# Performance work log

Hardware: AMD Instinct MI355X
Metric: run time of the kernel (lower is better)

Reference implementation:

```python
import jax, jax.numpy as jnp
import numpy as np

B, C, H, W = 16, 512, 64, 64


def setup_inputs() -> dict:
    key = jax.random.key(0)
    k1, k2 = jax.random.split(key)
    img_feat = jax.random.normal(k1, (B, C, H, W), dtype=jnp.float32)
    text_feat = jax.random.normal(k2, (B, C, H, W), dtype=jnp.float32)
    gamma = jnp.zeros((1,), dtype=jnp.float32)
    return {"img_feat": img_feat, "text_feat": text_feat, "gamma": gamma}


def reference(img_feat, text_feat, gamma):
    b, c, h, w = img_feat.shape
    q = img_feat.reshape(b, c, h * w)          # [B, C, HW]
    kv = text_feat.reshape(b, c, h * w)        # [B, C, HW]
    # channel-attention map: [B, C, C]
    attn = jnp.einsum('bcn,bdn->bcd', q, kv)
    attn = jax.nn.softmax(attn, axis=-1)
    info = jnp.einsum('bcd,bdn->bcn', attn, kv).reshape(b, c, h, w)
    return gamma * info + img_feat
```

## Files before the change

### kernel.cpp

```cpp
#include <hip/hip_runtime.h>
#include <hip/hip_bf16.h>


constexpr int NB = 16;
constexpr int NC = 512;
constexpr int NHW = 4096;
constexpr int QKSPLIT = 2;

typedef float f32x4 __attribute__((ext_vector_type(4)));
typedef __bf16 bf16x4 __attribute__((ext_vector_type(4)));
typedef __bf16 bf16x8 __attribute__((ext_vector_type(8)));

__device__ __forceinline__ void gload16(const void* g, void* l) {
  __builtin_amdgcn_global_load_lds(
      (const __attribute__((address_space(1))) void*)g,
      (__attribute__((address_space(3))) void*)l, 16, 0, 0);
}

template <int SPLITS>
__global__ __launch_bounds__(512) void gemm_qk(const float* __restrict__ Af,
                                               const __bf16* __restrict__ B,
                                               float* __restrict__ Dp) {
  __shared__ __bf16 sA[2][128 * 64];
  __shared__ __bf16 sB[2][128 * 64];

  const int t = threadIdx.x;
  const int lane = t & 63;
  const int wave = t >> 6;
  const int wr = wave >> 2;
  const int wc = wave & 3;

  constexpr int NWG = 16 * NB * SPLITS;
  constexpr int QX = NWG / 8;
  int flat = blockIdx.x + 4 * (blockIdx.y + 4 * blockIdx.z);
  flat = (flat & 7) * QX + (flat >> 3);
  const int bx = flat & 3;
  const int by = (flat >> 2) & 3;
  const int bz = flat >> 4;
  const int batch = bz / SPLITS;
  const int split = bz % SPLITS;

  const int aRow0 = bx * 128;
  const int bRow0 = by * 128;
  constexpr int KSUB = NHW / SPLITS;
  constexpr int NT = KSUB / 64;
  const int kBeg = split * KSUB;

  const int rl = lane >> 3;
  const int csrc = ((lane & 7) ^ rl) * 8;
  const __bf16* Bbase = B + (long)batch * NC * NHW +
                        (long)(bRow0 + wave * 16 + rl) * NHW + csrc + kBeg;
  const int ldsOff = wave * 16 * 64;

  const int c4 = (t & 15) * 4;
  const int rb = t >> 4;
  const float* Abase =
      Af + (long)batch * NC * NHW + (long)(aRow0 + rb) * NHW + kBeg + c4;

  f32x4 ra[4];
  auto loadA = [&](int kof) {
#pragma unroll
    for (int i = 0; i < 4; ++i)
      ra[i] = *(const f32x4*)(Abase + kof + (long)(32 * i) * NHW);
  };
  auto writeA = [&](int buf) {
#pragma unroll
    for (int i = 0; i < 4; ++i) {
      const int r = rb + 32 * i;
      const int idx = r * 64 + (c4 ^ ((r & 7) << 3));
      bf16x4 h = {(__bf16)ra[i].x, (__bf16)ra[i].y, (__bf16)ra[i].z,
                  (__bf16)ra[i].w};
      *(bf16x4*)&sA[buf][idx] = h;
    }
  };
  auto stageB = [&](int buf, int kof) {
#pragma unroll
    for (int i = 0; i < 2; ++i)
      gload16(Bbase + kof + (long)(i * 8) * NHW, &sB[buf][ldsOff + i * 8 * 64]);
  };

  f32x4 acc[4][2] = {};
  auto compute_tile = [&](int buf) {
#pragma unroll
    for (int kk = 0; kk < 2; ++kk) {
      const int kb = kk * 32 + ((lane >> 4) << 3);
      bf16x8 af[4], bfr[2];
#pragma unroll
      for (int m = 0; m < 4; ++m) {
        const int r = wr * 64 + m * 16 + (lane & 15);
        af[m] = *(const bf16x8*)&sA[buf][r * 64 + (kb ^ ((r & 7) << 3))];
      }
#pragma unroll
      for (int n = 0; n < 2; ++n) {
        const int r = wc * 32 + n * 16 + (lane & 15);
        bfr[n] = *(const bf16x8*)&sB[buf][r * 64 + (kb ^ ((r & 7) << 3))];
      }
#pragma unroll
      for (int m = 0; m < 4; ++m)
#pragma unroll
        for (int n = 0; n < 2; ++n)
          acc[m][n] = __builtin_amdgcn_mfma_f32_16x16x32_bf16(
              af[m], bfr[n], acc[m][n], 0, 0, 0);
    }
  };

  loadA(0);
  stageB(0, 0);
  asm volatile("s_waitcnt vmcnt(2)" ::: "memory");
  writeA(0);
  asm volatile("s_waitcnt vmcnt(0) lgkmcnt(0)" ::: "memory");
  __builtin_amdgcn_s_barrier();

  int cur = 0;
#pragma unroll 1
  for (int tt = 0; tt < NT; ++tt) {
    const bool more = (tt + 1) < NT;
    if (more) {
      loadA((tt + 1) * 64);
      stageB(cur ^ 1, (tt + 1) * 64);
      asm volatile("" ::: "memory");
    }
    compute_tile(cur);
    if (more) {
      asm volatile("s_waitcnt vmcnt(2)" ::: "memory");
      writeA(cur ^ 1);
      asm volatile("s_waitcnt vmcnt(0) lgkmcnt(0)" ::: "memory");
      __builtin_amdgcn_s_barrier();
      cur ^= 1;
    }
  }

  float* D = Dp + ((long)split * NB + batch) * NC * NC;
  const int m0 = aRow0 + wr * 64;
  const int n0 = bRow0 + wc * 32;
#pragma unroll
  for (int m = 0; m < 4; ++m)
#pragma unroll
    for (int n = 0; n < 2; ++n) {
      const int row0 = m0 + m * 16 + ((lane >> 4) << 2);
      const int col = n0 + n * 16 + (lane & 15);
#pragma unroll
      for (int r = 0; r < 4; ++r)
        D[(long)(row0 + r) * NC + col] = acc[m][n][r];
    }
}

__global__ __launch_bounds__(256) void gemm_pv(const __bf16* __restrict__ A,
                                               const __bf16* __restrict__ B,
                                               const float* __restrict__ img,
                                               const float* __restrict__ gammap,
                                               float* __restrict__ outp) {
  __shared__ __bf16 sA[64 * 64];
  __shared__ __bf16 sB[128 * 64];

  const int t = threadIdx.x;
  const int lane = t & 63;
  const int wave = t >> 6;
  const int wr = wave >> 1;
  const int wc = wave & 1;

  constexpr int GX = NHW / 64;
  constexpr int NWG = GX * 4 * NB;
  constexpr int QX = NWG / 8;
  int flat = blockIdx.x + GX * (blockIdx.y + 4 * blockIdx.z);
  flat = (flat & 7) * QX + (flat >> 3);
  const int bx = flat & 63;
  const int by = (flat >> 6) & 3;
  const int batch = flat >> 8;

  const int aRow0 = bx * 64;
  const int bRow0 = by * 128;

  const int rl = lane >> 3;
  const int csrc = ((lane & 7) ^ rl) * 8;
  const __bf16* Abase =
      A + (long)batch * NHW * NC + (long)(aRow0 + wave * 16 + rl) * NC + csrc;
  const int ldsOffA = wave * 16 * 64;
  const __bf16* Bbase =
      B + (long)batch * NC * NC + (long)(bRow0 + wave * 32 + rl) * NC + csrc;
  const int ldsOffB = wave * 32 * 64;

  f32x4 acc[2][4] = {};

#pragma unroll 1
  for (int k0 = 0; k0 < NC; k0 += 64) {
#pragma unroll
    for (int i = 0; i < 2; ++i)
      gload16(Abase + k0 + (long)(i * 8) * NC, &sA[ldsOffA + i * 8 * 64]);
#pragma unroll
    for (int i = 0; i < 4; ++i)
      gload16(Bbase + k0 + (long)(i * 8) * NC, &sB[ldsOffB + i * 8 * 64]);
    __syncthreads();
#pragma unroll
    for (int kk = 0; kk < 2; ++kk) {
      const int kb = kk * 32 + ((lane >> 4) << 3);
      bf16x8 af[2], bfr[4];
#pragma unroll
      for (int m = 0; m < 2; ++m) {
        const int r = wr * 32 + m * 16 + (lane & 15);
        af[m] = *(const bf16x8*)&sA[r * 64 + (kb ^ ((r & 7) << 3))];
      }
#pragma unroll
      for (int n = 0; n < 4; ++n) {
        const int r = wc * 64 + n * 16 + (lane & 15);
        bfr[n] = *(const bf16x8*)&sB[r * 64 + (kb ^ ((r & 7) << 3))];
      }
#pragma unroll
      for (int m = 0; m < 2; ++m)
#pragma unroll
        for (int n = 0; n < 4; ++n)
          acc[m][n] = __builtin_amdgcn_mfma_f32_16x16x32_bf16(
              af[m], bfr[n], acc[m][n], 0, 0, 0);
    }
    __syncthreads();
  }

  const float g = gammap[0];
  const long obase = (long)batch * NC * NHW;
  const int sp0 = aRow0 + wr * 32;
  const int ch0 = bRow0 + wc * 64;
#pragma unroll
  for (int m = 0; m < 2; ++m)
#pragma unroll
    for (int n = 0; n < 4; ++n) {
      const int sp = sp0 + m * 16 + ((lane >> 4) << 2);
      const int ch = ch0 + n * 16 + (lane & 15);
      const long idx = obase + (long)ch * NHW + sp;
      f32x4 iv = *(const f32x4*)(img + idx);
      f32x4 ov;
#pragma unroll
      for (int r = 0; r < 4; ++r) ov[r] = g * acc[m][n][r] + iv[r];
      *(f32x4*)(outp + idx) = ov;
    }
}

__global__ __launch_bounds__(256) void prep_kv(const float* __restrict__ kv,
                                               __bf16* __restrict__ kv16,
                                               __bf16* __restrict__ kvT) {
  __shared__ __bf16 tile[64 * 68];
  const int t = threadIdx.x;
  const int n0 = blockIdx.x * 64;
  const int d0 = blockIdx.y * 64;
  const long ibase = (long)blockIdx.z * NC * NHW;

  const int nc4 = (t & 15) * 4;
  const int dr0 = t >> 4;
#pragma unroll
  for (int i = 0; i < 4; ++i) {
    const int dr = dr0 + 16 * i;
    f32x4 v = *(const f32x4*)(kv + ibase + (long)(d0 + dr) * NHW + n0 + nc4);
    bf16x4 h = {(__bf16)v.x, (__bf16)v.y, (__bf16)v.z, (__bf16)v.w};
    *(bf16x4*)&tile[dr * 68 + nc4] = h;
    *(bf16x4*)(kv16 + ibase + (long)(d0 + dr) * NHW + n0 + nc4) = h;
  }
  __syncthreads();

  const long obase = (long)blockIdx.z * NHW * NC;
  const int nr = t >> 2;
  const int dc0 = t & 3;
#pragma unroll
  for (int i = 0; i < 2; ++i) {
    const int dc = dc0 + 4 * i;
    bf16x8 pk;
#pragma unroll
    for (int j = 0; j < 8; ++j) pk[j] = tile[(dc * 8 + j) * 68 + nr];
    *(bf16x8*)(kvT + obase + (long)(n0 + nr) * NC + d0 + dc * 8) = pk;
  }
}

template <int SPLITS>
__global__ __launch_bounds__(256) void softmax_rows(
    const float* __restrict__ attn, __bf16* __restrict__ P) {
  const int row = blockIdx.x * 4 + (threadIdx.x >> 6);
  const int lane = threadIdx.x & 63;
  const long PS = (long)NB * NC * NC;
  const float* src = attn + (long)row * NC;

  float x[8] = {0.f, 0.f, 0.f, 0.f, 0.f, 0.f, 0.f, 0.f};
#pragma unroll
  for (int s = 0; s < SPLITS; ++s) {
    f32x4 v0 = *(const f32x4*)(src + s * PS + lane * 4);
    f32x4 v1 = *(const f32x4*)(src + s * PS + 256 + lane * 4);
#pragma unroll
    for (int r = 0; r < 4; ++r) { x[r] += v0[r]; x[4 + r] += v1[r]; }
  }

  float mx = x[0];
#pragma unroll
  for (int r = 1; r < 8; ++r) mx = fmaxf(mx, x[r]);
#pragma unroll
  for (int off = 32; off >= 1; off >>= 1) mx = fmaxf(mx, __shfl_xor(mx, off));

  float e[8], s = 0.f;
#pragma unroll
  for (int r = 0; r < 8; ++r) { e[r] = __expf(x[r] - mx); s += e[r]; }
#pragma unroll
  for (int off = 32; off >= 1; off >>= 1) s += __shfl_xor(s, off);
  const float inv = 1.0f / s;

  __bf16* dst = P + (long)row * NC;
  bf16x4 h0, h1;
#pragma unroll
  for (int r = 0; r < 4; ++r) {
    h0[r] = (__bf16)(e[r] * inv);
    h1[r] = (__bf16)(e[4 + r] * inv);
  }
  *(bf16x4*)(dst + lane * 4) = h0;
  *(bf16x4*)(dst + 256 + lane * 4) = h1;
}

extern "C" void kernel_launch(void* const* d_in, const int* in_sizes, int n_in,
                              void* d_out, int out_size, void* d_ws,
                              size_t ws_size, hipStream_t stream) {
  const float* img = (const float*)d_in[0];
  const float* txt = (const float*)d_in[1];
  const float* gamma = (const float*)d_in[2];
  float* out = (float*)d_out;

  const size_t MiB = 1024 * 1024;
  __bf16* kv16 = (__bf16*)d_out;
  float* attnP = (float*)((char*)d_out + 68 * MiB);
  __bf16* kvT = (__bf16*)d_ws;
  __bf16* P = (__bf16*)((char*)d_ws + 64 * MiB);

  prep_kv<<<dim3(NHW / 64, NC / 64, NB), 256, 0, stream>>>(txt, kv16, kvT);

  gemm_qk<QKSPLIT><<<dim3(4, 4, NB * QKSPLIT), 512, 0, stream>>>(
      img, kv16, attnP);

  softmax_rows<QKSPLIT><<<dim3(NB * NC / 4), 256, 0, stream>>>(attnP, P);

  gemm_pv<<<dim3(NHW / 64, 4, NB), 256, 0, stream>>>(kvT, P, img, gamma, out);
}
```

Baseline: 233.0 us.

## Load PV GEMM operands directly from global into registers, dropping LDS staging

```diff
diff --git a/kernel.cpp b/kernel.cpp
--- a/kernel.cpp
+++ b/kernel.cpp
@@ -150,14 +150,11 @@
                                                const float* __restrict__ img,
                                                const float* __restrict__ gammap,
                                                float* __restrict__ outp) {
-  __shared__ __bf16 sA[64 * 64];
-  __shared__ __bf16 sB[128 * 64];
-
   const int t = threadIdx.x;
   const int lane = t & 63;
   const int wave = t >> 6;
-  const int wr = wave >> 1;
-  const int wc = wave & 1;
+  const int wsp = wave >> 1;
+  const int wch = wave & 1;
 
   constexpr int GX = NHW / 64;
   constexpr int NWG = GX * 4 * NB;
@@ -171,54 +168,43 @@
   const int aRow0 = bx * 64;
   const int bRow0 = by * 128;
 
-  const int rl = lane >> 3;
-  const int csrc = ((lane & 7) ^ rl) * 8;
-  const __bf16* Abase =
-      A + (long)batch * NHW * NC + (long)(aRow0 + wave * 16 + rl) * NC + csrc;
-  const int ldsOffA = wave * 16 * 64;
-  const __bf16* Bbase =
-      B + (long)batch * NC * NC + (long)(bRow0 + wave * 32 + rl) * NC + csrc;
-  const int ldsOffB = wave * 32 * 64;
+  const int rl = lane & 15;
+  const int kl = (lane >> 4) * 8;
+
+  const __bf16* Ab0 =
+      A + (long)batch * NHW * NC + (long)(aRow0 + wsp * 32 + rl) * NC + kl;
+  const __bf16* Ab1 = Ab0 + 16 * NC;
+  const __bf16* Bb0 =
+      B + (long)batch * NC * NC + (long)(bRow0 + wch * 64 + rl) * NC + kl;
+  const __bf16* Bb1 = Bb0 + 16 * NC;
+  const __bf16* Bb2 = Bb0 + 32 * NC;
+  const __bf16* Bb3 = Bb0 + 48 * NC;
 
   f32x4 acc[2][4] = {};
 
-#pragma unroll 1
-  for (int k0 = 0; k0 < NC; k0 += 64) {
-#pragma unroll
-    for (int i = 0; i < 2; ++i)
-      gload16(Abase + k0 + (long)(i * 8) * NC, &sA[ldsOffA + i * 8 * 64]);
-#pragma unroll
-    for (int i = 0; i < 4; ++i)
-      gload16(Bbase + k0 + (long)(i * 8) * NC, &sB[ldsOffB + i * 8 * 64]);
-    __syncthreads();
-#pragma unroll
-    for (int kk = 0; kk < 2; ++kk) {
-      const int kb = kk * 32 + ((lane >> 4) << 3);
-      bf16x8 af[2], bfr[4];
-#pragma unroll
-      for (int m = 0; m < 2; ++m) {
-        const int r = wr * 32 + m * 16 + (lane & 15);
-        af[m] = *(const bf16x8*)&sA[r * 64 + (kb ^ ((r & 7) << 3))];
-      }
-#pragma unroll
-      for (int n = 0; n < 4; ++n) {
-        const int r = wc * 64 + n * 16 + (lane & 15);
-        bfr[n] = *(const bf16x8*)&sB[r * 64 + (kb ^ ((r & 7) << 3))];
-      }
-#pragma unroll
-      for (int m = 0; m < 2; ++m)
-#pragma unroll
-        for (int n = 0; n < 4; ++n)
-          acc[m][n] = __builtin_amdgcn_mfma_f32_16x16x32_bf16(
-              af[m], bfr[n], acc[m][n], 0, 0, 0);
-    }
-    __syncthreads();
+#pragma unroll
+  for (int ks = 0; ks < 16; ++ks) {
+    const int ko = ks * 32;
+    bf16x8 a0 = *(const bf16x8*)(Ab0 + ko);
+    bf16x8 a1 = *(const bf16x8*)(Ab1 + ko);
+    bf16x8 b0 = *(const bf16x8*)(Bb0 + ko);
+    bf16x8 b1 = *(const bf16x8*)(Bb1 + ko);
+    bf16x8 b2 = *(const bf16x8*)(Bb2 + ko);
+    bf16x8 b3 = *(const bf16x8*)(Bb3 + ko);
+    acc[0][0] = __builtin_amdgcn_mfma_f32_16x16x32_bf16(a0, b0, acc[0][0], 0, 0, 0);
+    acc[0][1] = __builtin_amdgcn_mfma_f32_16x16x32_bf16(a0, b1, acc[0][1], 0, 0, 0);
+    acc[0][2] = __builtin_amdgcn_mfma_f32_16x16x32_bf16(a0, b2, acc[0][2], 0, 0, 0);
+    acc[0][3] = __builtin_amdgcn_mfma_f32_16x16x32_bf16(a0, b3, acc[0][3], 0, 0, 0);
+    acc[1][0] = __builtin_amdgcn_mfma_f32_16x16x32_bf16(a1, b0, acc[1][0], 0, 0, 0);
+    acc[1][1] = __builtin_amdgcn_mfma_f32_16x16x32_bf16(a1, b1, acc[1][1], 0, 0, 0);
+    acc[1][2] = __builtin_amdgcn_mfma_f32_16x16x32_bf16(a1, b2, acc[1][2], 0, 0, 0);
+    acc[1][3] = __builtin_amdgcn_mfma_f32_16x16x32_bf16(a1, b3, acc[1][3], 0, 0, 0);
   }
 
   const float g = gammap[0];
   const long obase = (long)batch * NC * NHW;
-  const int sp0 = aRow0 + wr * 32;
-  const int ch0 = bRow0 + wc * 64;
+  const int sp0 = aRow0 + wsp * 32;
+  const int ch0 = bRow0 + wch * 64;
 #pragma unroll
   for (int m = 0; m < 2; ++m)
 #pragma unroll
```

After: 339.9 us. +45.9%, slower.
